# Kernel tuning notes

Measured on AMD Instinct MI355X. Metric: run time of the kernel, lower is better.

## Reference

```python
import jax, jax.numpy as jnp
import numpy as np

N, E, D = 50000, 500000, 128


def layer_norm(x, w, b, eps=1e-5):
    mu = jnp.mean(x, axis=-1, keepdims=True)
    var = jnp.var(x, axis=-1, keepdims=True)
    return (x - mu) * jax.lax.rsqrt(var + eps) * w + b


def setup_inputs() -> dict:
    key = jax.random.key(0)
    ks = jax.random.split(key, 8)
    z = jax.random.normal(ks[0], (N, D), dtype=jnp.float32)
    pot_arcs = jax.random.randint(ks[1], (E, 2), 0, N, dtype=jnp.int64)
    s = 1.0 / np.sqrt(D)
    lin1_w = jax.random.uniform(ks[2], (D, D), jnp.float32, -s, s)
    lin1_b = jax.random.uniform(ks[3], (D,), jnp.float32, -s, s)
    lin2_w = jax.random.uniform(ks[4], (D, D), jnp.float32, -s, s)
    lin2_b = jax.random.uniform(ks[5], (D,), jnp.float32, -s, s)
    bil_w = jax.random.uniform(ks[6], (1, D, D), jnp.float32, -s, s)
    bil_b = jax.random.uniform(ks[7], (1,), jnp.float32, -s, s)
    norm_w = jnp.ones((D,), jnp.float32)
    norm_b = jnp.zeros((D,), jnp.float32)
    return {"z": z, "pot_arcs": pot_arcs, "lin1_w": lin1_w, "lin1_b": lin1_b,
            "lin2_w": lin2_w, "lin2_b": lin2_b, "bil_w": bil_w, "bil_b": bil_b,
            "norm_w": norm_w, "norm_b": norm_b}


def reference(z, pot_arcs, lin1_w, lin1_b, lin2_w, lin2_b, bil_w, bil_b, norm_w, norm_b):
    # shared LayerNorm on all nodes
    zn = layer_norm(z, norm_w, norm_b)                     # [N, D]
    x1 = zn[pot_arcs[:, 0]]                                # [E, D] gather heads
    x2 = zn[pot_arcs[:, 1]]                                # [E, D] gather tails
    # lin -> relu -> layernorm (dropout = identity at eval)
    h1 = layer_norm(jax.nn.relu(x1 @ lin1_w.T + lin1_b), norm_w, norm_b)
    h2 = layer_norm(jax.nn.relu(x2 @ lin2_w.T + lin2_b), norm_w, norm_b)
    # bilinear score: out_e = h1_e^T W h2_e + b, W = bil_w[0]
    score = jnp.einsum('ed,df,ef->e', h1, bil_w[0], h2) + bil_b[0]
    return score                                           # [E]
```

## Files before the change

kernel.cpp:

```cpp
#include <hip/hip_runtime.h>

#define D 128
#define TM 64

typedef __attribute__((ext_vector_type(8))) short short8v;
typedef __attribute__((ext_vector_type(4))) float float4v;

__device__ __forceinline__ unsigned short f2bf(float f) {
    unsigned int u = __float_as_uint(f);
    u += 0x7FFFu + ((u >> 16) & 1u);
    return (unsigned short)(u >> 16);
}
__device__ __forceinline__ float bflo(int u) {
    return __uint_as_float(((unsigned int)u) << 16);
}
__device__ __forceinline__ float bfhi(int u) {
    return __uint_as_float(((unsigned int)u) & 0xFFFF0000u);
}

__global__ __launch_bounds__(256) void wconv(
    const float* __restrict__ w1, const float* __restrict__ w2,
    const float* __restrict__ wb, unsigned short* __restrict__ dst)
{
    int tid = blockIdx.x * 256 + threadIdx.x;
    int w = tid >> 11;
    int r = tid & 2047;
    int l = r & 63;
    int tk = r >> 6;
    int t = tk >> 2, ks = tk & 3;
    int n = t * 16 + (l & 15);
    int k = ks * 32 + (l >> 4) * 8;
    const float* src = (w == 0) ? w1 : (w == 1) ? w2 : wb;
    const float* p = src + n * D + k;
    float4 a = *(const float4*)p;
    float4 b = *(const float4*)(p + 4);
    union { int4 i4; unsigned short u[8]; } pk;
    pk.u[0] = f2bf(a.x); pk.u[1] = f2bf(a.y); pk.u[2] = f2bf(a.z); pk.u[3] = f2bf(a.w);
    pk.u[4] = f2bf(b.x); pk.u[5] = f2bf(b.y); pk.u[6] = f2bf(b.z); pk.u[7] = f2bf(b.w);
    *(int4*)(dst + (size_t)tid * 8) = pk.i4;
}

__global__ __launch_bounds__(256) void node_kernel(
    const float* __restrict__ z,
    const unsigned short* __restrict__ wfrag,
    const float* __restrict__ lin1_b, const float* __restrict__ lin2_b,
    const float* __restrict__ norm_w, const float* __restrict__ norm_b,
    unsigned short* __restrict__ T1, unsigned short* __restrict__ T2,
    int N)
{
    __shared__ unsigned short sa[TM][136];
    __shared__ unsigned short sh[TM][136];

    const int tid   = threadIdx.x;
    const int lane  = tid & 63;
    const int wave  = tid >> 6;
    const int n0    = blockIdx.x * TM;
    const int cg    = lane & 15;
    const int q     = lane >> 4;
    const int rbase = wave * 16;

    {
        const int c = cg * 8;
        float4 nw0 = *(const float4*)(norm_w + c);
        float4 nw1 = *(const float4*)(norm_w + c + 4);
        float4 nb0 = *(const float4*)(norm_b + c);
        float4 nb1 = *(const float4*)(norm_b + c + 4);
        #pragma unroll
        for (int it = 0; it < 4; ++it) {
            int rr = rbase + it * 4 + q;
            int n  = n0 + rr;
            int nc = (n < N) ? n : (N - 1);
            const float* zp = z + (size_t)nc * D + c;
            float4 v0 = *(const float4*)zp;
            float4 v1 = *(const float4*)(zp + 4);
            float s  = v0.x + v0.y + v0.z + v0.w + v1.x + v1.y + v1.z + v1.w;
            float qq = v0.x*v0.x + v0.y*v0.y + v0.z*v0.z + v0.w*v0.w
                     + v1.x*v1.x + v1.y*v1.y + v1.z*v1.z + v1.w*v1.w;
            #pragma unroll
            for (int m = 1; m <= 8; m <<= 1) {
                s  += __shfl_xor(s, m, 64);
                qq += __shfl_xor(qq, m, 64);
            }
            float mu  = s * (1.0f / D);
            float var = qq * (1.0f / D) - mu * mu;
            float rs  = rsqrtf(var + 1e-5f);
            union { int4 i4; unsigned short u[8]; } pk;
            pk.u[0] = f2bf((v0.x - mu) * rs * nw0.x + nb0.x);
            pk.u[1] = f2bf((v0.y - mu) * rs * nw0.y + nb0.y);
            pk.u[2] = f2bf((v0.z - mu) * rs * nw0.z + nb0.z);
            pk.u[3] = f2bf((v0.w - mu) * rs * nw0.w + nb0.w);
            pk.u[4] = f2bf((v1.x - mu) * rs * nw1.x + nb1.x);
            pk.u[5] = f2bf((v1.y - mu) * rs * nw1.y + nb1.y);
            pk.u[6] = f2bf((v1.z - mu) * rs * nw1.z + nb1.z);
            pk.u[7] = f2bf((v1.w - mu) * rs * nw1.w + nb1.w);
            *(int4*)&sa[rr][c] = pk.i4;
        }
    }

    float4v acc1[8], acc2[8];
    #pragma unroll
    for (int t = 0; t < 8; ++t) { acc1[t] = (float4v)(0.0f); acc2[t] = (float4v)(0.0f); }
    #pragma unroll
    for (int ks = 0; ks < 4; ++ks) {
        short8v a = *(const short8v*)&sa[rbase + cg][ks * 32 + q * 8];
        const short8v* wp = (const short8v*)wfrag + ks * 64 + lane;
        #pragma unroll
        for (int t = 0; t < 8; ++t) {
            acc1[t] = __builtin_amdgcn_mfma_f32_16x16x32_bf16(a, wp[t * 256],        acc1[t], 0, 0, 0);
            acc2[t] = __builtin_amdgcn_mfma_f32_16x16x32_bf16(a, wp[t * 256 + 2048], acc2[t], 0, 0, 0);
        }
    }

    float nwv[8], nbv[8];
    #pragma unroll
    for (int t = 0; t < 8; ++t) {
        nwv[t] = norm_w[t * 16 + cg];
        nbv[t] = norm_b[t * 16 + cg];
    }

    auto epilogue = [&](float4v* acc, const float* lb, unsigned short (*dst)[136]) {
        float s[4] = {0, 0, 0, 0}, qs[4] = {0, 0, 0, 0};
        #pragma unroll
        for (int t = 0; t < 8; ++t) {
            float b = lb[t * 16 + cg];
            #pragma unroll
            for (int i = 0; i < 4; ++i) {
                float v = fmaxf(acc[t][i] + b, 0.0f);
                acc[t][i] = v;
                s[i] += v; qs[i] += v * v;
            }
        }
        #pragma unroll
        for (int i = 0; i < 4; ++i) {
            #pragma unroll
            for (int m = 1; m <= 8; m <<= 1) {
                s[i]  += __shfl_xor(s[i], m, 64);
                qs[i] += __shfl_xor(qs[i], m, 64);
            }
            float mu  = s[i] * (1.0f / D);
            float var = qs[i] * (1.0f / D) - mu * mu;
            s[i] = mu; qs[i] = rsqrtf(var + 1e-5f);
        }
        #pragma unroll
        for (int t = 0; t < 8; ++t) {
            #pragma unroll
            for (int i = 0; i < 4; ++i)
                dst[rbase + q * 4 + i][t * 16 + cg] = f2bf((acc[t][i] - s[i]) * qs[i] * nwv[t] + nbv[t]);
        }
    };

    auto copyout = [&](const unsigned short (*S)[136], unsigned short* dst) {
        int r = rbase + (lane >> 2);
        int n = n0 + r;
        if (n < N) {
            #pragma unroll
            for (int j = 0; j < 4; ++j) {
                int c = (lane & 3) * 8 + j * 32;
                *(int4*)(dst + (size_t)n * D + c) = *(const int4*)&S[r][c];
            }
        }
    };

    epilogue(acc1, lin1_b, sh);
    epilogue(acc2, lin2_b, sa);
    copyout(sh, T1);

    #pragma unroll
    for (int t = 0; t < 8; ++t) acc1[t] = (float4v)(0.0f);
    #pragma unroll
    for (int ks = 0; ks < 4; ++ks) {
        short8v a = *(const short8v*)&sa[rbase + cg][ks * 32 + q * 8];
        const short8v* wp = (const short8v*)wfrag + 4096 + ks * 64 + lane;
        #pragma unroll
        for (int t = 0; t < 8; ++t)
            acc1[t] = __builtin_amdgcn_mfma_f32_16x16x32_bf16(a, wp[t * 256], acc1[t], 0, 0, 0);
    }
    #pragma unroll
    for (int t = 0; t < 8; ++t)
        #pragma unroll
        for (int i = 0; i < 4; ++i)
            sh[rbase + q * 4 + i][t * 16 + cg] = f2bf(acc1[t][i]);
    copyout(sh, T2);
}

__global__ __launch_bounds__(256) void arc_kernel(
    const int* __restrict__ arcs,
    const unsigned short* __restrict__ T1,
    const unsigned short* __restrict__ T2,
    const float* __restrict__ bil_b,
    float* __restrict__ out, int E)
{
    const int tid  = threadIdx.x;
    const int lane = tid & 63;
    long long gw = ((long long)blockIdx.x * 256 + tid) >> 6;
    long long e0 = gw * 32;
    int aidx = lane >> 2;
    int s    = lane & 3;

    long long ii = e0 * 2 + lane;
    long long iimax = (long long)E * 2 - 1;
    int iv = arcs[ii <= iimax ? ii : iimax];
    int a0A = __shfl(iv, aidx * 2, 64);
    int a1A = __shfl(iv, aidx * 2 + 1, 64);
    int a0B = __shfl(iv, 32 + aidx * 2, 64);
    int a1B = __shfl(iv, 32 + aidx * 2 + 1, 64);

    const int4* PA = (const int4*)(T1 + (size_t)a0A * D);
    const int4* QA = (const int4*)(T2 + (size_t)a1A * D);
    const int4* PB = (const int4*)(T1 + (size_t)a0B * D);
    const int4* QB = (const int4*)(T2 + (size_t)a1B * D);

    int4 xA0 = PA[s];      int4 xA1 = PA[s + 4];
    int4 xA2 = PA[s + 8];  int4 xA3 = PA[s + 12];
    int4 yA0 = QA[s];      int4 yA1 = QA[s + 4];
    int4 yA2 = QA[s + 8];  int4 yA3 = QA[s + 12];
    int4 xB0 = PB[s];      int4 xB1 = PB[s + 4];
    int4 xB2 = PB[s + 8];  int4 xB3 = PB[s + 12];
    int4 yB0 = QB[s];      int4 yB1 = QB[s + 4];
    int4 yB2 = QB[s + 8];  int4 yB3 = QB[s + 12];

    auto dot16 = [](int4 x0, int4 x1, int4 x2, int4 x3,
                    int4 y0, int4 y1, int4 y2, int4 y3) -> float {
        float acc = 0.0f;
        acc += bflo(x0.x)*bflo(y0.x) + bfhi(x0.x)*bfhi(y0.x);
        acc += bflo(x0.y)*bflo(y0.y) + bfhi(x0.y)*bfhi(y0.y);
        acc += bflo(x0.z)*bflo(y0.z) + bfhi(x0.z)*bfhi(y0.z);
        acc += bflo(x0.w)*bflo(y0.w) + bfhi(x0.w)*bfhi(y0.w);
        acc += bflo(x1.x)*bflo(y1.x) + bfhi(x1.x)*bfhi(y1.x);
        acc += bflo(x1.y)*bflo(y1.y) + bfhi(x1.y)*bfhi(y1.y);
        acc += bflo(x1.z)*bflo(y1.z) + bfhi(x1.z)*bfhi(y1.z);
        acc += bflo(x1.w)*bflo(y1.w) + bfhi(x1.w)*bfhi(y1.w);
        acc += bflo(x2.x)*bflo(y2.x) + bfhi(x2.x)*bfhi(y2.x);
        acc += bflo(x2.y)*bflo(y2.y) + bfhi(x2.y)*bfhi(y2.y);
        acc += bflo(x2.z)*bflo(y2.z) + bfhi(x2.z)*bfhi(y2.z);
        acc += bflo(x2.w)*bflo(y2.w) + bfhi(x2.w)*bfhi(y2.w);
        acc += bflo(x3.x)*bflo(y3.x) + bfhi(x3.x)*bfhi(y3.x);
        acc += bflo(x3.y)*bflo(y3.y) + bfhi(x3.y)*bfhi(y3.y);
        acc += bflo(x3.z)*bflo(y3.z) + bfhi(x3.z)*bfhi(y3.z);
        acc += bflo(x3.w)*bflo(y3.w) + bfhi(x3.w)*bfhi(y3.w);
        return acc;
    };

    float accA = dot16(xA0, xA1, xA2, xA3, yA0, yA1, yA2, yA3);
    float accB = dot16(xB0, xB1, xB2, xB3, yB0, yB1, yB2, yB3);

    accA += __shfl_xor(accA, 1, 64);
    accA += __shfl_xor(accA, 2, 64);
    accB += __shfl_xor(accB, 1, 64);
    accB += __shfl_xor(accB, 2, 64);

    if (s == 0) {
        float bb = bil_b[0];
        long long eA = e0 + aidx;
        long long eB = e0 + 16 + aidx;
        if (eA < E) out[eA] = accA + bb;
        if (eB < E) out[eB] = accB + bb;
    }
}

extern "C" void kernel_launch(void* const* d_in, const int* in_sizes, int n_in,
                              void* d_out, int out_size, void* d_ws, size_t ws_size,
                              hipStream_t stream) {
    const float* z      = (const float*)d_in[0];
    const int*   arcs   = (const int*)d_in[1];
    const float* lin1_w = (const float*)d_in[2];
    const float* lin1_b = (const float*)d_in[3];
    const float* lin2_w = (const float*)d_in[4];
    const float* lin2_b = (const float*)d_in[5];
    const float* bil_w  = (const float*)d_in[6];
    const float* bil_b  = (const float*)d_in[7];
    const float* norm_w = (const float*)d_in[8];
    const float* norm_b = (const float*)d_in[9];
    float* out = (float*)d_out;

    const int N = in_sizes[0] / D;
    const int E = in_sizes[1] / 2;

    unsigned short* wfrag = (unsigned short*)d_ws;
    unsigned short* T1 = wfrag + 3 * 16384;
    unsigned short* T2 = T1 + (size_t)N * D;

    wconv<<<24, 256, 0, stream>>>(lin1_w, lin2_w, bil_w, wfrag);

    node_kernel<<<(N + TM - 1) / TM, 256, 0, stream>>>(
        z, wfrag, lin1_b, lin2_b, norm_w, norm_b, T1, T2, N);

    long long waves = ((long long)E + 31) / 32;
    int blocks = (int)((waves + 3) / 4);
    arc_kernel<<<blocks, 256, 0, stream>>>(arcs, T1, T2, bil_b, out, E);
}
```

Measured before the change: 140.5 us.

## Double node tile per block and reuse weight fragments across two row tiles

The node kernel now handles 128 rows per block, with each wave owning two 16-row MFMA tiles that share every loaded weight fragment. The three GEMMs run one after another, and the second LDS buffer is removed. Epilogues now write 2-byte bf16 elements straight to global memory instead of staging through LDS for coalesced 16-byte copies. The goal is to halve weight-fragment loads per row and cut LDS use. The cost is scattered 2-byte global stores, fewer blocks in the grid, and more accumulator registers.

```diff
diff --git a/kernel.cpp b/kernel.cpp
--- a/kernel.cpp
+++ b/kernel.cpp
@@ -1,7 +1,7 @@
 #include <hip/hip_runtime.h>
 
 #define D 128
-#define TM 64
+#define TM 128
 
 typedef __attribute__((ext_vector_type(8))) short short8v;
 typedef __attribute__((ext_vector_type(4))) float float4v;
@@ -49,7 +49,6 @@
     int N)
 {
     __shared__ unsigned short sa[TM][136];
-    __shared__ unsigned short sh[TM][136];
 
     const int tid   = threadIdx.x;
     const int lane  = tid & 63;
@@ -57,7 +56,8 @@
     const int n0    = blockIdx.x * TM;
     const int cg    = lane & 15;
     const int q     = lane >> 4;
-    const int rbase = wave * 16;
+    const int rb0   = wave * 32;
+    const int rb1   = rb0 + 16;
 
     {
         const int c = cg * 8;
@@ -66,8 +66,8 @@
         float4 nb0 = *(const float4*)(norm_b + c);
         float4 nb1 = *(const float4*)(norm_b + c + 4);
         #pragma unroll
-        for (int it = 0; it < 4; ++it) {
-            int rr = rbase + it * 4 + q;
+        for (int it = 0; it < 8; ++it) {
+            int rr = rb0 + it * 4 + q;
             int n  = n0 + rr;
             int nc = (n < N) ? n : (N - 1);
             const float* zp = z + (size_t)nc * D + c;
@@ -97,28 +97,26 @@
         }
     }
 
-    float4v acc1[8], acc2[8];
-    #pragma unroll
-    for (int t = 0; t < 8; ++t) { acc1[t] = (float4v)(0.0f); acc2[t] = (float4v)(0.0f); }
-    #pragma unroll
-    for (int ks = 0; ks < 4; ++ks) {
-        short8v a = *(const short8v*)&sa[rbase + cg][ks * 32 + q * 8];
-        const short8v* wp = (const short8v*)wfrag + ks * 64 + lane;
-        #pragma unroll
-        for (int t = 0; t < 8; ++t) {
-            acc1[t] = __builtin_amdgcn_mfma_f32_16x16x32_bf16(a, wp[t * 256],        acc1[t], 0, 0, 0);
-            acc2[t] = __builtin_amdgcn_mfma_f32_16x16x32_bf16(a, wp[t * 256 + 2048], acc2[t], 0, 0, 0);
-        }
-    }
-
-    float nwv[8], nbv[8];
-    #pragma unroll
-    for (int t = 0; t < 8; ++t) {
-        nwv[t] = norm_w[t * 16 + cg];
-        nbv[t] = norm_b[t * 16 + cg];
-    }
-
-    auto epilogue = [&](float4v* acc, const float* lb, unsigned short (*dst)[136]) {
+    auto gemm_dual = [&](int wofs, float4v (&acc)[2][8]) {
+        #pragma unroll
+        for (int m = 0; m < 2; ++m)
+            #pragma unroll
+            for (int t = 0; t < 8; ++t) acc[m][t] = (float4v)(0.0f);
+        #pragma unroll
+        for (int ks = 0; ks < 4; ++ks) {
+            short8v aA = *(const short8v*)&sa[rb0 + cg][ks * 32 + q * 8];
+            short8v aB = *(const short8v*)&sa[rb1 + cg][ks * 32 + q * 8];
+            const short8v* wp = (const short8v*)wfrag + wofs + ks * 64 + lane;
+            #pragma unroll
+            for (int t = 0; t < 8; ++t) {
+                short8v b = wp[t * 256];
+                acc[0][t] = __builtin_amdgcn_mfma_f32_16x16x32_bf16(aA, b, acc[0][t], 0, 0, 0);
+                acc[1][t] = __builtin_amdgcn_mfma_f32_16x16x32_bf16(aB, b, acc[1][t], 0, 0, 0);
+            }
+        }
+    };
+
+    auto ln_stats = [&](float4v* acc, const float* lb, float* mu, float* rs) {
         float s[4] = {0, 0, 0, 0}, qs[4] = {0, 0, 0, 0};
         #pragma unroll
         for (int t = 0; t < 8; ++t) {
@@ -137,50 +135,67 @@
                 s[i]  += __shfl_xor(s[i], m, 64);
                 qs[i] += __shfl_xor(qs[i], m, 64);
             }
-            float mu  = s[i] * (1.0f / D);
-            float var = qs[i] * (1.0f / D) - mu * mu;
-            s[i] = mu; qs[i] = rsqrtf(var + 1e-5f);
-        }
+            float muv = s[i] * (1.0f / D);
+            float var = qs[i] * (1.0f / D) - muv * muv;
+            mu[i] = muv; rs[i] = rsqrtf(var + 1e-5f);
+        }
+    };
+
+    auto epi_global = [&](float4v* acc, const float* lb, int rbm, unsigned short* dst) {
+        float mu[4], rs[4];
+        ln_stats(acc, lb, mu, rs);
         #pragma unroll
         for (int t = 0; t < 8; ++t) {
+            int col = t * 16 + cg;
+            float nw = norm_w[col], nb = norm_b[col];
+            #pragma unroll
+            for (int i = 0; i < 4; ++i) {
+                int n = n0 + rbm + q * 4 + i;
+                if (n < N)
+                    dst[(size_t)n * D + col] = f2bf((acc[t][i] - mu[i]) * rs[i] * nw + nb);
+            }
+        }
+    };
+
+    auto epi_lds = [&](float4v* acc, const float* lb, int rbm) {
+        float mu[4], rs[4];
+        ln_stats(acc, lb, mu, rs);
+        #pragma unroll
+        for (int t = 0; t < 8; ++t) {
+            int col = t * 16 + cg;
+            float nw = norm_w[col], nb = norm_b[col];
             #pragma unroll
             for (int i = 0; i < 4; ++i)
-                dst[rbase + q * 4 + i][t * 16 + cg] = f2bf((acc[t][i] - s[i]) * qs[i] * nwv[t] + nbv[t]);
-        }
-    };
-
-    auto copyout = [&](const unsigned short (*S)[136], unsigned short* dst) {
-        int r = rbase + (lane >> 2);
-        int n = n0 + r;
-        if (n < N) {
-            #pragma unroll
-            for (int j = 0; j < 4; ++j) {
-                int c = (lane & 3) * 8 + j * 32;
-                *(int4*)(dst + (size_t)n * D + c) = *(const int4*)&S[r][c];
-            }
-        }
-    };
-
-    epilogue(acc1, lin1_b, sh);
-    epilogue(acc2, lin2_b, sa);
-    copyout(sh, T1);
-
-    #pragma unroll
-    for (int t = 0; t < 8; ++t) acc1[t] = (float4v)(0.0f);
-    #pragma unroll
-    for (int ks = 0; ks < 4; ++ks) {
-        short8v a = *(const short8v*)&sa[rbase + cg][ks * 32 + q * 8];
-        const short8v* wp = (const short8v*)wfrag + 4096 + ks * 64 + lane;
-        #pragma unroll
-        for (int t = 0; t < 8; ++t)
-            acc1[t] = __builtin_amdgcn_mfma_f32_16x16x32_bf16(a, wp[t * 256], acc1[t], 0, 0, 0);
-    }
-    #pragma unroll
-    for (int t = 0; t < 8; ++t)
-        #pragma unroll
-        for (int i = 0; i < 4; ++i)
-            sh[rbase + q * 4 + i][t * 16 + cg] = f2bf(acc1[t][i]);
-    copyout(sh, T2);
+                sa[rbm + q * 4 + i][col] = f2bf((acc[t][i] - mu[i]) * rs[i] * nw + nb);
+        }
+    };
+
+    auto raw_store = [&](float4v* acc, int rbm, unsigned short* dst) {
+        #pragma unroll
+        for (int t = 0; t < 8; ++t) {
+            int col = t * 16 + cg;
+            #pragma unroll
+            for (int i = 0; i < 4; ++i) {
+                int n = n0 + rbm + q * 4 + i;
+                if (n < N)
+                    dst[(size_t)n * D + col] = f2bf(acc[t][i]);
+            }
+        }
+    };
+
+    float4v acc[2][8];
+
+    gemm_dual(0, acc);
+    epi_global(acc[0], lin1_b, rb0, T1);
+    epi_global(acc[1], lin1_b, rb1, T1);
+
+    gemm_dual(2048, acc);
+    epi_lds(acc[0], lin2_b, rb0);
+    epi_lds(acc[1], lin2_b, rb1);
+
+    gemm_dual(4096, acc);
+    raw_store(acc[0], rb0, T2);
+    raw_store(acc[1], rb1, T2);
 }
 
 __global__ __launch_bounds__(256) void arc_kernel(
```

Result: slower. 159.9 us (+13.9%).

## Split node kernel output columns across two wave groups with cross-wave LayerNorm reduction

Applied to the files above, without the earlier changes.

The node kernel now runs 512 threads per block, and two wave groups each compute half of the 128 output columns for the same 16-row slices. This halves the accumulator registers per wave and raises parallelism. Row statistics for the post-ReLU LayerNorm are combined through a small shared-memory buffer with extra barriers. The shared staging tile for outputs is dropped, so T1 and T2 are written directly as scattered 2-byte global stores instead of coalesced 16-byte copies, which may cost store efficiency.

```diff
diff --git a/kernel.cpp b/kernel.cpp
--- a/kernel.cpp
+++ b/kernel.cpp
@@ -40,7 +40,7 @@
     *(int4*)(dst + (size_t)tid * 8) = pk.i4;
 }
 
-__global__ __launch_bounds__(256) void node_kernel(
+__global__ __launch_bounds__(512) void node_kernel(
     const float* __restrict__ z,
     const unsigned short* __restrict__ wfrag,
     const float* __restrict__ lin1_b, const float* __restrict__ lin2_b,
@@ -49,15 +49,17 @@
     int N)
 {
     __shared__ unsigned short sa[TM][136];
-    __shared__ unsigned short sh[TM][136];
+    __shared__ float sred[2][TM][4];
 
     const int tid   = threadIdx.x;
     const int lane  = tid & 63;
     const int wave  = tid >> 6;
+    const int g     = wave & 3;
+    const int th    = wave >> 2;
     const int n0    = blockIdx.x * TM;
     const int cg    = lane & 15;
     const int q     = lane >> 4;
-    const int rbase = wave * 16;
+    const int rbase = g * 16;
 
     {
         const int c = cg * 8;
@@ -66,8 +68,8 @@
         float4 nb0 = *(const float4*)(norm_b + c);
         float4 nb1 = *(const float4*)(norm_b + c + 4);
         #pragma unroll
-        for (int it = 0; it < 4; ++it) {
-            int rr = rbase + it * 4 + q;
+        for (int it = 0; it < 2; ++it) {
+            int rr = wave * 8 + it * 4 + q;
             int n  = n0 + rr;
             int nc = (n < N) ? n : (N - 1);
             const float* zp = z + (size_t)nc * D + c;
@@ -96,91 +98,115 @@
             *(int4*)&sa[rr][c] = pk.i4;
         }
     }
-
-    float4v acc1[8], acc2[8];
-    #pragma unroll
-    for (int t = 0; t < 8; ++t) { acc1[t] = (float4v)(0.0f); acc2[t] = (float4v)(0.0f); }
+    __syncthreads();
+
+    float4v acc1[4], acc2[4];
+    #pragma unroll
+    for (int t0 = 0; t0 < 4; ++t0) { acc1[t0] = (float4v)(0.0f); acc2[t0] = (float4v)(0.0f); }
     #pragma unroll
     for (int ks = 0; ks < 4; ++ks) {
         short8v a = *(const short8v*)&sa[rbase + cg][ks * 32 + q * 8];
         const short8v* wp = (const short8v*)wfrag + ks * 64 + lane;
         #pragma unroll
-        for (int t = 0; t < 8; ++t) {
-            acc1[t] = __builtin_amdgcn_mfma_f32_16x16x32_bf16(a, wp[t * 256],        acc1[t], 0, 0, 0);
-            acc2[t] = __builtin_amdgcn_mfma_f32_16x16x32_bf16(a, wp[t * 256 + 2048], acc2[t], 0, 0, 0);
-        }
-    }
-
-    float nwv[8], nbv[8];
-    #pragma unroll
-    for (int t = 0; t < 8; ++t) {
-        nwv[t] = norm_w[t * 16 + cg];
-        nbv[t] = norm_b[t * 16 + cg];
-    }
-
-    auto epilogue = [&](float4v* acc, const float* lb, unsigned short (*dst)[136]) {
-        float s[4] = {0, 0, 0, 0}, qs[4] = {0, 0, 0, 0};
-        #pragma unroll
-        for (int t = 0; t < 8; ++t) {
-            float b = lb[t * 16 + cg];
-            #pragma unroll
-            for (int i = 0; i < 4; ++i) {
-                float v = fmaxf(acc[t][i] + b, 0.0f);
-                acc[t][i] = v;
-                s[i] += v; qs[i] += v * v;
-            }
-        }
+        for (int t0 = 0; t0 < 4; ++t0) {
+            int t = th * 4 + t0;
+            acc1[t0] = __builtin_amdgcn_mfma_f32_16x16x32_bf16(a, wp[t * 256],        acc1[t0], 0, 0, 0);
+            acc2[t0] = __builtin_amdgcn_mfma_f32_16x16x32_bf16(a, wp[t * 256 + 2048], acc2[t0], 0, 0, 0);
+        }
+    }
+
+    float s1[4] = {0,0,0,0}, q1[4] = {0,0,0,0};
+    float s2[4] = {0,0,0,0}, q2[4] = {0,0,0,0};
+    #pragma unroll
+    for (int t0 = 0; t0 < 4; ++t0) {
+        int col = (th * 4 + t0) * 16 + cg;
+        float b1 = lin1_b[col];
+        float b2 = lin2_b[col];
         #pragma unroll
         for (int i = 0; i < 4; ++i) {
-            #pragma unroll
-            for (int m = 1; m <= 8; m <<= 1) {
-                s[i]  += __shfl_xor(s[i], m, 64);
-                qs[i] += __shfl_xor(qs[i], m, 64);
-            }
-            float mu  = s[i] * (1.0f / D);
-            float var = qs[i] * (1.0f / D) - mu * mu;
-            s[i] = mu; qs[i] = rsqrtf(var + 1e-5f);
-        }
-        #pragma unroll
-        for (int t = 0; t < 8; ++t) {
-            #pragma unroll
-            for (int i = 0; i < 4; ++i)
-                dst[rbase + q * 4 + i][t * 16 + cg] = f2bf((acc[t][i] - s[i]) * qs[i] * nwv[t] + nbv[t]);
-        }
-    };
-
-    auto copyout = [&](const unsigned short (*S)[136], unsigned short* dst) {
-        int r = rbase + (lane >> 2);
-        int n = n0 + r;
-        if (n < N) {
-            #pragma unroll
-            for (int j = 0; j < 4; ++j) {
-                int c = (lane & 3) * 8 + j * 32;
-                *(int4*)(dst + (size_t)n * D + c) = *(const int4*)&S[r][c];
-            }
-        }
-    };
-
-    epilogue(acc1, lin1_b, sh);
-    epilogue(acc2, lin2_b, sa);
-    copyout(sh, T1);
-
-    #pragma unroll
-    for (int t = 0; t < 8; ++t) acc1[t] = (float4v)(0.0f);
+            float v1 = fmaxf(acc1[t0][i] + b1, 0.0f);
+            float v2 = fmaxf(acc2[t0][i] + b2, 0.0f);
+            acc1[t0][i] = v1; acc2[t0][i] = v2;
+            s1[i] += v1; q1[i] += v1 * v1;
+            s2[i] += v2; q2[i] += v2 * v2;
+        }
+    }
+    #pragma unroll
+    for (int i = 0; i < 4; ++i) {
+        #pragma unroll
+        for (int m = 1; m <= 8; m <<= 1) {
+            s1[i] += __shfl_xor(s1[i], m, 64);
+            q1[i] += __shfl_xor(q1[i], m, 64);
+            s2[i] += __shfl_xor(s2[i], m, 64);
+            q2[i] += __shfl_xor(q2[i], m, 64);
+        }
+    }
+    if (cg == 0) {
+        #pragma unroll
+        for (int i = 0; i < 4; ++i) {
+            int row = rbase + q * 4 + i;
+            sred[th][row][0] = s1[i]; sred[th][row][1] = q1[i];
+            sred[th][row][2] = s2[i]; sred[th][row][3] = q2[i];
+        }
+    }
+    __syncthreads();
+
+    float mu1[4], rs1[4], mu2[4], rs2[4];
+    #pragma unroll
+    for (int i = 0; i < 4; ++i) {
+        int row = rbase + q * 4 + i;
+        float ts1 = s1[i] + sred[1 - th][row][0];
+        float tq1 = q1[i] + sred[1 - th][row][1];
+        float ts2 = s2[i] + sred[1 - th][row][2];
+        float tq2 = q2[i] + sred[1 - th][row][3];
+        mu1[i] = ts1 * (1.0f / D);
+        rs1[i] = rsqrtf(tq1 * (1.0f / D) - mu1[i] * mu1[i] + 1e-5f);
+        mu2[i] = ts2 * (1.0f / D);
+        rs2[i] = rsqrtf(tq2 * (1.0f / D) - mu2[i] * mu2[i] + 1e-5f);
+    }
+
+    #pragma unroll
+    for (int t0 = 0; t0 < 4; ++t0) {
+        int col = (th * 4 + t0) * 16 + cg;
+        float nw = norm_w[col], nb = norm_b[col];
+        #pragma unroll
+        for (int i = 0; i < 4; ++i) {
+            int n = n0 + rbase + q * 4 + i;
+            if (n < N)
+                T1[(size_t)n * D + col] = f2bf((acc1[t0][i] - mu1[i]) * rs1[i] * nw + nb);
+        }
+    }
+    #pragma unroll
+    for (int t0 = 0; t0 < 4; ++t0) {
+        int col = (th * 4 + t0) * 16 + cg;
+        float nw = norm_w[col], nb = norm_b[col];
+        #pragma unroll
+        for (int i = 0; i < 4; ++i)
+            sa[rbase + q * 4 + i][col] = f2bf((acc2[t0][i] - mu2[i]) * rs2[i] * nw + nb);
+    }
+    __syncthreads();
+
+    float4v acc3[4];
+    #pragma unroll
+    for (int t0 = 0; t0 < 4; ++t0) acc3[t0] = (float4v)(0.0f);
     #pragma unroll
     for (int ks = 0; ks < 4; ++ks) {
         short8v a = *(const short8v*)&sa[rbase + cg][ks * 32 + q * 8];
         const short8v* wp = (const short8v*)wfrag + 4096 + ks * 64 + lane;
         #pragma unroll
-        for (int t = 0; t < 8; ++t)
-            acc1[t] = __builtin_amdgcn_mfma_f32_16x16x32_bf16(a, wp[t * 256], acc1[t], 0, 0, 0);
-    }
-    #pragma unroll
-    for (int t = 0; t < 8; ++t)
-        #pragma unroll
-        for (int i = 0; i < 4; ++i)
-            sh[rbase + q * 4 + i][t * 16 + cg] = f2bf(acc1[t][i]);
-    copyout(sh, T2);
+        for (int t0 = 0; t0 < 4; ++t0)
+            acc3[t0] = __builtin_amdgcn_mfma_f32_16x16x32_bf16(a, wp[(th * 4 + t0) * 256], acc3[t0], 0, 0, 0);
+    }
+    #pragma unroll
+    for (int t0 = 0; t0 < 4; ++t0) {
+        int col = (th * 4 + t0) * 16 + cg;
+        #pragma unroll
+        for (int i = 0; i < 4; ++i) {
+            int n = n0 + rbase + q * 4 + i;
+            if (n < N)
+                T2[(size_t)n * D + col] = f2bf(acc3[t0][i]);
+        }
+    }
 }
 
 __global__ __launch_bounds__(256) void arc_kernel(
@@ -282,7 +308,7 @@
 
     wconv<<<24, 256, 0, stream>>>(lin1_w, lin2_w, bil_w, wfrag);
 
-    node_kernel<<<(N + TM - 1) / TM, 256, 0, stream>>>(
+    node_kernel<<<(N + TM - 1) / TM, 512, 0, stream>>>(
         z, wfrag, lin1_b, lin2_b, norm_w, norm_b, T1, T2, N);
 
     long long waves = ((long long)E + 31) / 32;
```

New measurement: 144.8 us. 3.1% more time.
